# Kernel tuning notes

Measured on AMD Instinct MI355X. Metric: run time of the kernel, lower is better.

## Reference

```python
import jax, jax.numpy as jnp
import numpy as np

RHO = 1e-8
EPS = 1e-8
THRESH = 0.9
MARK = -2


def maxi(x):
    # keep only the max entry along last dim, zero elsewhere
    idx = jnp.argmax(x, axis=-1, keepdims=True)
    return jnp.where(jnp.arange(x.shape[-1]) == idx, x, 0.0)


def argmaxi(x, eps=EPS):
    mx = jnp.abs(maxi(x))
    factors = jnp.max(mx, axis=-1, keepdims=True) - eps
    return mx / factors


def outer_forward(mm0, xs, rho=RHO):
    # mm0: (fields, mems, dim), xs: (batch, fields, dim)
    m = mm0 - 0.5
    x = xs - 0.5
    num = jnp.einsum('fmd,bfd->bfm', m, x) * 0.5
    m_norm = jnp.sqrt(jnp.sum(m * m, axis=-1))            # (f, m)
    x_norm = jnp.sqrt(jnp.sum(x * x, axis=-1))[..., None]  # (b, f, 1)
    return num / (m_norm[None] * x_norm + rho) + 0.5


def hidden_forward(mm, child_x, rho=RHO):
    # mm: (nodes, children, h_mems, c_mems), child_x: (batch, nodes*children, c_mems)
    n, c, hm, cm = mm.shape
    b = child_x.shape[0]
    x = maxi(child_x).reshape(b, n, c, cm)
    prop = jnp.einsum('nchk,bnck->bnh', mm, x)
    x_norm = jnp.sqrt(jnp.sum(x * x, axis=(2, 3)))[..., None]  # (b, n, 1)
    return prop / (c * x_norm + rho)


def mark_reserved_indices(acts, usages, trigger, mark=MARK):
    # acts: (b, n, m); usages: (n, m); trigger: (b, n, 1)
    res = jnp.argsort(acts, axis=-1)[:, :, -1:]        # argmax index, (b, n, 1)
    res = jnp.where(trigger, -1, res)
    res = res[:, :, 0].T                               # (n, b)
    sort_indices = jnp.argsort(usages, axis=-1)        # (n, m) ascending usage
    mask = res != -1                                   # (n, b)
    matches = ((res[:, :, None] == sort_indices[:, None, :]) & mask[:, :, None]).any(axis=1)  # (n, m)
    return jnp.where(matches, mark, sort_indices), sort_indices


def move_value_to_back(x, value=MARK):
    order = jnp.argsort((x == value).astype(jnp.int32), axis=-1)  # stable sort
    return jnp.take_along_axis(x, order, axis=-1)


def expand_for_batches(x, batch_size):
    n, m = x.shape
    full = batch_size // m + 1
    tiled = jnp.broadcast_to(x[None], (full, n, m)).transpose(1, 0, 2).reshape(n, -1)
    return tiled[:, :batch_size]


def growth_argmaxi(x, counts, eps=EPS, threshold=THRESH):
    b, n, m = x.shape
    normal = argmaxi(x, eps)
    trigger = jnp.sum(x > threshold, axis=-1, keepdims=True) <= 0  # (b, n, 1)
    avail, allidx = mark_reserved_indices(normal, counts, trigger, MARK)
    avail = move_value_to_back(avail, MARK)
    avail = expand_for_batches(avail, b)
    allidx = expand_for_batches(allidx, b)
    final = jnp.where(avail == MARK, allidx, avail)  # (n, b)
    idx = final.T.reshape(b, n, 1)
    vals = jnp.take_along_axis(x, idx, axis=-1)
    vals = jnp.where(vals == 0, 1.0, vals)
    gp = jnp.where(jnp.arange(m) == idx, vals, 0.0)  # scatter into zeros
    gp = argmaxi(jnp.abs(gp), eps)
    grown = jnp.where(trigger, gp, normal)
    uc = jnp.sum(grown, axis=0)
    uc = jnp.where(uc <= 0, counts, uc)
    return grown, uc


def setup_inputs() -> dict:
    key = jax.random.key(0)
    k1, k2, k3, k4 = jax.random.split(key, 4)
    xs = jax.random.uniform(k1, (32, 4096, 64), dtype=jnp.float32)
    mm0 = jax.random.uniform(k2, (4096, 64, 64), dtype=jnp.float32)
    mm1 = jax.random.normal(k3, (512, 8, 64, 64), dtype=jnp.float32) * 0.1
    mm2 = jax.random.normal(k4, (64, 8, 64, 64), dtype=jnp.float32) * 0.1
    counts = jnp.ones((64, 64), dtype=jnp.float32)
    return {'xs': xs, 'mm0': mm0, 'mm1': mm1, 'mm2': mm2, 'counts': counts}


def reference(xs, mm0, mm1, mm2, counts):
    h0 = outer_forward(mm0, xs)      # (b, 4096, 64)
    h1 = hidden_forward(mm1, h0)     # (b, 512, 64)
    h2 = hidden_forward(mm2, h1)     # (b, 64, 64)
    grown, _ = growth_argmaxi(h2, counts)
    return grown
```

## Files before the change

### kernel.cpp

```cpp
#include <hip/hip_runtime.h>
#include <cstdint>
#include <cstddef>

#define RHO 1e-8f
#define EPSV 1e-8f
#define THRESH 0.9f

typedef float v2f __attribute__((ext_vector_type(2)));

__device__ __forceinline__ float wave_max(float v) {
#pragma unroll
  for (int off = 1; off < 64; off <<= 1) v = fmaxf(v, __shfl_xor(v, off, 64));
  return v;
}

__global__ __launch_bounds__(128) void stage1_kernel(
    const float* __restrict__ xs, const float* __restrict__ mm0,
    float* __restrict__ maxv1, int* __restrict__ idx1) {
  const int lane = threadIdx.x & 63;
  const int wave = threadIdx.x >> 6;
  const int f = __builtin_amdgcn_readfirstlane(blockIdx.x * 2 + wave);

  __shared__ float vbuf[2][32 * 65];
  float* vb = vbuf[wave];

  const float4* mrow =
      reinterpret_cast<const float4*>(mm0 + ((size_t)f * 64 + lane) * 64);
  v2f m2[32];
#pragma unroll
  for (int j = 0; j < 16; ++j) {
    float4 v = mrow[j];
    m2[2 * j] = (v2f){v.x - 0.5f, v.y - 0.5f};
    m2[2 * j + 1] = (v2f){v.z - 0.5f, v.w - 0.5f};
  }
  v2f mn2 = {0.f, 0.f}, sm2 = {0.f, 0.f};
#pragma unroll
  for (int j = 0; j < 32; ++j) {
    mn2 = m2[j] * m2[j] + mn2;
    sm2 = sm2 + m2[j];
  }
  const float mn = sqrtf(mn2.x + mn2.y);
  const float sm = sm2.x + sm2.y;

  float xnv;
  {
    const int b = lane & 31;
    const float4* xr =
        reinterpret_cast<const float4*>(xs + ((size_t)b * 4096 + f) * 64);
    v2f s2 = {0.f, 0.f}, s1 = {0.f, 0.f};
#pragma unroll
    for (int j = 0; j < 16; ++j) {
      float4 v = xr[j];
      v2f p0 = {v.x, v.y}, p1 = {v.z, v.w};
      s2 = p0 * p0 + s2;
      s2 = p1 * p1 + s2;
      s1 = s1 + p0 + p1;
    }
    xnv = sqrtf(s2.x + s2.y - (s1.x + s1.y) + 16.f);
  }

  const float* xf = xs + (size_t)f * 64;
#pragma clang loop unroll_count(1)
  for (int b = 0; b < 32; ++b) {
    const float4* xq = reinterpret_cast<const float4*>(xf + (size_t)b * (4096 * 64));
    const float xnb =
        __int_as_float(__builtin_amdgcn_readlane(__float_as_int(xnv), b));
    v2f a0 = {0.f, 0.f}, a1 = {0.f, 0.f}, a2 = {0.f, 0.f}, a3 = {0.f, 0.f};
#pragma unroll
    for (int j = 0; j < 16; j += 4) {
      float4 q0 = xq[j], q1 = xq[j + 1], q2 = xq[j + 2], q3 = xq[j + 3];
      a0 = m2[2 * j + 0] * (v2f){q0.x, q0.y} + a0;
      a0 = m2[2 * j + 1] * (v2f){q0.z, q0.w} + a0;
      a1 = m2[2 * j + 2] * (v2f){q1.x, q1.y} + a1;
      a1 = m2[2 * j + 3] * (v2f){q1.z, q1.w} + a1;
      a2 = m2[2 * j + 4] * (v2f){q2.x, q2.y} + a2;
      a2 = m2[2 * j + 5] * (v2f){q2.z, q2.w} + a2;
      a3 = m2[2 * j + 6] * (v2f){q3.x, q3.y} + a3;
      a3 = m2[2 * j + 7] * (v2f){q3.z, q3.w} + a3;
    }
    v2f as = (a0 + a1) + (a2 + a3);
    const float acc = as.x + as.y - 0.5f * sm;
    const float val = (acc * 0.5f) / (mn * xnb + RHO) + 0.5f;
    vb[b * 65 + lane] = val;
  }

  const int bb = lane & 31, half = lane >> 5;
  float best = -__builtin_inff();
  int bi = 0;
#pragma unroll
  for (int j = 0; j < 32; ++j) {
    float v = vb[bb * 65 + half * 32 + j];
    if (v > best) { best = v; bi = half * 32 + j; }
  }
  const float ov = __shfl_xor(best, 32, 64);
  const int oi = __shfl_xor(bi, 32, 64);
  const bool lo = (half == 0);
  const float bl = lo ? best : ov;
  const int il = lo ? bi : oi;
  const float bh = lo ? ov : best;
  const int ih = lo ? oi : bi;
  const float fb = (bl >= bh) ? bl : bh;
  const int fi = (bl >= bh) ? il : ih;
  if (lane < 32) {
    maxv1[f * 32 + lane] = fb;
    idx1[f * 32 + lane] = fi;
  }
}

__global__ __launch_bounds__(256) void stage2_kernel(
    const float* __restrict__ maxv_in, const int* __restrict__ idx_in,
    const float* __restrict__ mm,
    float* __restrict__ maxv_out, int* __restrict__ idx_out) {
  const int node = blockIdx.x;
  const int lane = threadIdx.x & 63;
  const int wave = threadIdx.x >> 6;
  const int tid = threadIdx.x;

  __shared__ float tile[4 * 4096];

  const float4* src = reinterpret_cast<const float4*>(mm + (size_t)node * (8 * 4096));

  float acc[8], s2[8];
#pragma unroll
  for (int i = 0; i < 8; ++i) { acc[i] = 0.f; s2[i] = 0.f; }

#pragma clang loop unroll_count(1)
  for (int phase = 0; phase < 2; ++phase) {
    if (phase) __syncthreads();
#pragma unroll
    for (int i = 0; i < 16; ++i) {
      int g = tid + 256 * i;
      float4 v = src[phase * 4096 + g];
      int cl = g >> 10, rem = g & 1023;
      int h = rem >> 4, k0 = (rem & 15) * 4;
      float* base = &tile[cl * 4096];
      base[(k0 + 0) * 64 + (h ^ (k0 + 0))] = v.x;
      base[(k0 + 1) * 64 + (h ^ (k0 + 1))] = v.y;
      base[(k0 + 2) * 64 + (h ^ (k0 + 2))] = v.z;
      base[(k0 + 3) * 64 + (h ^ (k0 + 3))] = v.w;
    }
    __syncthreads();
#pragma unroll
    for (int i = 0; i < 8; ++i) {
      const int b = wave * 8 + i;
#pragma unroll
      for (int cl = 0; cl < 4; ++cl) {
        const int c = phase * 4 + cl;
        const int off = __builtin_amdgcn_readfirstlane((node * 8 + c) * 32 + b);
        const int k = idx_in[off];
        const float v = maxv_in[off];
        const float w = tile[cl * 4096 + k * 64 + (lane ^ k)];
        acc[i] = fmaf(w, v, acc[i]);
        s2[i] = fmaf(v, v, s2[i]);
      }
    }
  }

#pragma unroll
  for (int i = 0; i < 8; ++i) {
    const int b = wave * 8 + i;
    const float val = acc[i] / (8.f * sqrtf(s2[i]) + RHO);
    const float mx = wave_max(val);
    unsigned long long t = __ballot(val == mx);
    int j0 = __ffsll((long long)t) - 1;
    if (lane == 0) {
      maxv_out[node * 32 + b] = mx;
      idx_out[node * 32 + b] = j0;
    }
  }
}

__global__ __launch_bounds__(256) void grow_kernel(
    const float* __restrict__ maxv_in, const int* __restrict__ idx_in,
    const float* __restrict__ mm,
    const float* __restrict__ counts, float* __restrict__ out) {
  const int node = blockIdx.x;
  const int lane = threadIdx.x & 63;
  const int wave = threadIdx.x >> 6;
  const int tid = threadIdx.x;

  __shared__ float tile[2 * 4096];
  __shared__ float hbuf[32 * 64];
  __shared__ float mxvS[32];
  __shared__ int idxS[32];
  __shared__ int trgS[32];
  __shared__ float cntS[64];
  __shared__ int sidxS[64];
  __shared__ int flagS[64];
  __shared__ int compS[64];
  __shared__ int selS[32];
  __shared__ float valS[32];
  __shared__ int keptS[1];

  const float4* src = reinterpret_cast<const float4*>(mm + (size_t)node * (8 * 4096));

  float acc[8], s2[8];
#pragma unroll
  for (int i = 0; i < 8; ++i) { acc[i] = 0.f; s2[i] = 0.f; }

#pragma clang loop unroll_count(1)
  for (int phase = 0; phase < 4; ++phase) {
    if (phase) __syncthreads();
#pragma unroll
    for (int i = 0; i < 8; ++i) {
      int g = tid + 256 * i;
      float4 v = src[phase * 2048 + g];
      int cl = g >> 10, rem = g & 1023;
      int h = rem >> 4, k0 = (rem & 15) * 4;
      float* base = &tile[cl * 4096];
      base[(k0 + 0) * 64 + (h ^ (k0 + 0))] = v.x;
      base[(k0 + 1) * 64 + (h ^ (k0 + 1))] = v.y;
      base[(k0 + 2) * 64 + (h ^ (k0 + 2))] = v.z;
      base[(k0 + 3) * 64 + (h ^ (k0 + 3))] = v.w;
    }
    __syncthreads();
#pragma unroll
    for (int i = 0; i < 8; ++i) {
      const int b = wave * 8 + i;
#pragma unroll
      for (int cl = 0; cl < 2; ++cl) {
        const int c = phase * 2 + cl;
        const int off = __builtin_amdgcn_readfirstlane((node * 8 + c) * 32 + b);
        const int k = idx_in[off];
        const float v = maxv_in[off];
        const float w = tile[cl * 4096 + k * 64 + (lane ^ k)];
        acc[i] = fmaf(w, v, acc[i]);
        s2[i] = fmaf(v, v, s2[i]);
      }
    }
  }

#pragma unroll
  for (int i = 0; i < 8; ++i) {
    const int b = wave * 8 + i;
    const float val = acc[i] / (8.f * sqrtf(s2[i]) + RHO);
    const float mx = wave_max(val);
    unsigned long long t = __ballot(val == mx);
    int j0 = __ffsll((long long)t) - 1;
    hbuf[b * 64 + lane] = val;
    unsigned long long big = __ballot(val > THRESH);
    if (lane == 0) {
      mxvS[b] = mx; idxS[b] = j0; trgS[b] = (big == 0ULL) ? 1 : 0;
    }
  }

  if (tid < 64) { cntS[tid] = counts[node * 64 + tid]; flagS[tid] = 0; }
  __syncthreads();
  if (tid < 64) {
    float cl = cntS[tid];
    int rank = 0;
    for (int j = 0; j < 64; ++j) {
      float cj = cntS[j];
      rank += (cj < cl || (cj == cl && j < tid)) ? 1 : 0;
    }
    sidxS[rank] = tid;
  }
  __syncthreads();
  if (tid < 32) {
    const int b = tid;
    if (!trgS[b]) {
      int j = idxS[b];
      float a = fabsf(mxvS[b]);
      int res;
      if (a > EPSV) res = j;
      else if (a == 0.f) res = 63;
      else if (a == EPSV) res = j;
      else res = (j == 63) ? 62 : 63;
      flagS[res] = 1;
    }
  }
  __syncthreads();
  if (wave == 0) {
    int s = sidxS[lane];
    int keep = flagS[s] ? 0 : 1;
    unsigned long long kb = __ballot(keep);
    int pos = __popcll(kb & ((1ULL << lane) - 1ULL));
    if (keep) compS[pos] = s;
    if (lane == 0) keptS[0] = __popcll(kb);
  }
  __syncthreads();
  if (tid < 32) {
    const int b = tid;
    int fin = (b < keptS[0]) ? compS[b] : sidxS[b];
    int idxb; float a;
    if (trgS[b]) {
      idxb = fin;
      float v = hbuf[b * 64 + idxb];
      if (v == 0.f) v = 1.f;
      a = fabsf(v);
    } else {
      idxb = idxS[b];
      a = fabsf(mxvS[b]);
    }
    selS[b] = idxb;
    valS[b] = a / (a - EPSV);
  }
  __syncthreads();
#pragma unroll
  for (int r = 0; r < 8; ++r) {
    int i = tid + 256 * r;
    int b = i >> 6, h = i & 63;
    out[((size_t)b * 64 + node) * 64 + h] = (h == selS[b]) ? valS[b] : 0.f;
  }
}

extern "C" void kernel_launch(void* const* d_in, const int* in_sizes, int n_in,
                              void* d_out, int out_size, void* d_ws, size_t ws_size,
                              hipStream_t stream) {
  const float* xs = (const float*)d_in[0];
  const float* mm0 = (const float*)d_in[1];
  const float* mm1 = (const float*)d_in[2];
  const float* mm2 = (const float*)d_in[3];
  const float* counts = (const float*)d_in[4];
  float* out = (float*)d_out;
  char* ws = (char*)d_ws;

  float* maxv1 = (float*)(ws + 0);
  int* idx1 = (int*)(ws + 524288);
  float* maxv2 = (float*)(ws + 1048576);
  int* idx2 = (int*)(ws + 1114112);

  stage1_kernel<<<dim3(2048), dim3(128), 0, stream>>>(xs, mm0, maxv1, idx1);
  stage2_kernel<<<dim3(512), dim3(256), 0, stream>>>(maxv1, idx1, mm1, maxv2, idx2);
  grow_kernel<<<dim3(64), dim3(256), 0, stream>>>(maxv2, idx2, mm2, counts, out);
}
```

Measured before the change: 225.2 us.

## Stage stage1 operands in LDS with register-tiled outer product; double-buffer child tiles

Stage1 now loads each field's centered memory matrix and batch vectors into padded shared memory and computes the 64x32 dot products as an 8x4 register-tiled outer product per lane, followed by a shuffle-based argmax reduction. Before, each lane held one memory row in registers and streamed every batch row from global memory. In stage2 and grow, the per-node weight staging is reworked into a register-prefetched ping-pong between two LDS tiles, one child at a time, so global loads overlap compute. The costs are higher register pressure from the 64-accumulator tile, extra LDS traffic, and a changed tie-break and precision path, since inputs are now centered before the norm is computed.

```diff
diff --git a/kernel.cpp b/kernel.cpp
--- a/kernel.cpp
+++ b/kernel.cpp
@@ -21,91 +21,153 @@
   const int wave = threadIdx.x >> 6;
   const int f = __builtin_amdgcn_readfirstlane(blockIdx.x * 2 + wave);
 
-  __shared__ float vbuf[2][32 * 65];
-  float* vb = vbuf[wave];
-
-  const float4* mrow =
-      reinterpret_cast<const float4*>(mm0 + ((size_t)f * 64 + lane) * 64);
-  v2f m2[32];
-#pragma unroll
-  for (int j = 0; j < 16; ++j) {
-    float4 v = mrow[j];
-    m2[2 * j] = (v2f){v.x - 0.5f, v.y - 0.5f};
-    m2[2 * j + 1] = (v2f){v.z - 0.5f, v.w - 0.5f};
-  }
-  v2f mn2 = {0.f, 0.f}, sm2 = {0.f, 0.f};
-#pragma unroll
-  for (int j = 0; j < 32; ++j) {
-    mn2 = m2[j] * m2[j] + mn2;
-    sm2 = sm2 + m2[j];
-  }
-  const float mn = sqrtf(mn2.x + mn2.y);
-  const float sm = sm2.x + sm2.y;
-
-  float xnv;
+  __shared__ float mbuf[2][64 * 68];
+  __shared__ float xbuf[2][32 * 68];
+  float* mb = mbuf[wave];
+  float* xb = xbuf[wave];
+
+  const float* mf = mm0 + (size_t)f * 4096;
+#pragma unroll
+  for (int i = 0; i < 16; ++i) {
+    const int g = i * 64 + lane;
+    const int r = g >> 4, dq = g & 15;
+    float4 v = *reinterpret_cast<const float4*>(mf + r * 64 + dq * 4);
+    float4 w = {v.x - 0.5f, v.y - 0.5f, v.z - 0.5f, v.w - 0.5f};
+    *reinterpret_cast<float4*>(&mb[r * 68 + dq * 4]) = w;
+  }
+  const float* xf = xs + (size_t)f * 64;
+#pragma unroll
+  for (int i = 0; i < 8; ++i) {
+    const int g = i * 64 + lane;
+    const int b = g >> 4, dq = g & 15;
+    float4 v = *reinterpret_cast<const float4*>(xf + (size_t)b * (4096 * 64) + dq * 4);
+    float4 w = {v.x - 0.5f, v.y - 0.5f, v.z - 0.5f, v.w - 0.5f};
+    *reinterpret_cast<float4*>(&xb[b * 68 + dq * 4]) = w;
+  }
+
+  float mnv, xnv;
   {
-    const int b = lane & 31;
-    const float4* xr =
-        reinterpret_cast<const float4*>(xs + ((size_t)b * 4096 + f) * 64);
-    v2f s2 = {0.f, 0.f}, s1 = {0.f, 0.f};
+    v2f s = {0.f, 0.f};
+    const float* mr = &mb[lane * 68];
 #pragma unroll
     for (int j = 0; j < 16; ++j) {
-      float4 v = xr[j];
-      v2f p0 = {v.x, v.y}, p1 = {v.z, v.w};
-      s2 = p0 * p0 + s2;
-      s2 = p1 * p1 + s2;
-      s1 = s1 + p0 + p1;
-    }
-    xnv = sqrtf(s2.x + s2.y - (s1.x + s1.y) + 16.f);
-  }
-
-  const float* xf = xs + (size_t)f * 64;
-#pragma clang loop unroll_count(1)
-  for (int b = 0; b < 32; ++b) {
-    const float4* xq = reinterpret_cast<const float4*>(xf + (size_t)b * (4096 * 64));
-    const float xnb =
-        __int_as_float(__builtin_amdgcn_readlane(__float_as_int(xnv), b));
-    v2f a0 = {0.f, 0.f}, a1 = {0.f, 0.f}, a2 = {0.f, 0.f}, a3 = {0.f, 0.f};
-#pragma unroll
-    for (int j = 0; j < 16; j += 4) {
-      float4 q0 = xq[j], q1 = xq[j + 1], q2 = xq[j + 2], q3 = xq[j + 3];
-      a0 = m2[2 * j + 0] * (v2f){q0.x, q0.y} + a0;
-      a0 = m2[2 * j + 1] * (v2f){q0.z, q0.w} + a0;
-      a1 = m2[2 * j + 2] * (v2f){q1.x, q1.y} + a1;
-      a1 = m2[2 * j + 3] * (v2f){q1.z, q1.w} + a1;
-      a2 = m2[2 * j + 4] * (v2f){q2.x, q2.y} + a2;
-      a2 = m2[2 * j + 5] * (v2f){q2.z, q2.w} + a2;
-      a3 = m2[2 * j + 6] * (v2f){q3.x, q3.y} + a3;
-      a3 = m2[2 * j + 7] * (v2f){q3.z, q3.w} + a3;
-    }
-    v2f as = (a0 + a1) + (a2 + a3);
-    const float acc = as.x + as.y - 0.5f * sm;
-    const float val = (acc * 0.5f) / (mn * xnb + RHO) + 0.5f;
-    vb[b * 65 + lane] = val;
-  }
-
-  const int bb = lane & 31, half = lane >> 5;
-  float best = -__builtin_inff();
-  int bi = 0;
-#pragma unroll
-  for (int j = 0; j < 32; ++j) {
-    float v = vb[bb * 65 + half * 32 + j];
-    if (v > best) { best = v; bi = half * 32 + j; }
-  }
-  const float ov = __shfl_xor(best, 32, 64);
-  const int oi = __shfl_xor(bi, 32, 64);
-  const bool lo = (half == 0);
-  const float bl = lo ? best : ov;
-  const int il = lo ? bi : oi;
-  const float bh = lo ? ov : best;
-  const int ih = lo ? oi : bi;
-  const float fb = (bl >= bh) ? bl : bh;
-  const int fi = (bl >= bh) ? il : ih;
-  if (lane < 32) {
-    maxv1[f * 32 + lane] = fb;
-    idx1[f * 32 + lane] = fi;
-  }
-}
+      float4 v = *reinterpret_cast<const float4*>(mr + 4 * j);
+      s = (v2f){v.x, v.y} * (v2f){v.x, v.y} + s;
+      s = (v2f){v.z, v.w} * (v2f){v.z, v.w} + s;
+    }
+    mnv = sqrtf(s.x + s.y);
+  }
+  {
+    v2f s = {0.f, 0.f};
+    const float* xr = &xb[(lane & 31) * 68];
+#pragma unroll
+    for (int j = 0; j < 16; ++j) {
+      float4 v = *reinterpret_cast<const float4*>(xr + 4 * j);
+      s = (v2f){v.x, v.y} * (v2f){v.x, v.y} + s;
+      s = (v2f){v.z, v.w} * (v2f){v.z, v.w} + s;
+    }
+    xnv = sqrtf(s.x + s.y);
+  }
+
+  const int mg = lane >> 3, bg = lane & 7;
+  v2f acc[8][4][2];
+#pragma unroll
+  for (int i = 0; i < 8; ++i)
+#pragma unroll
+    for (int j = 0; j < 4; ++j) {
+      acc[i][j][0] = (v2f){0.f, 0.f};
+      acc[i][j][1] = (v2f){0.f, 0.f};
+    }
+
+#pragma unroll
+  for (int d0 = 0; d0 < 64; d0 += 4) {
+    float4 a[8], bx[4];
+#pragma unroll
+    for (int i = 0; i < 8; ++i)
+      a[i] = *reinterpret_cast<const float4*>(&mb[(mg + 8 * i) * 68 + d0]);
+#pragma unroll
+    for (int j = 0; j < 4; ++j)
+      bx[j] = *reinterpret_cast<const float4*>(&xb[(bg + 8 * j) * 68 + d0]);
+#pragma unroll
+    for (int i = 0; i < 8; ++i)
+#pragma unroll
+      for (int j = 0; j < 4; ++j) {
+        acc[i][j][0] = (v2f){a[i].x, a[i].y} * (v2f){bx[j].x, bx[j].y} + acc[i][j][0];
+        acc[i][j][1] = (v2f){a[i].z, a[i].w} * (v2f){bx[j].z, bx[j].w} + acc[i][j][1];
+      }
+  }
+
+  float mn_i[8], xn_j[4];
+#pragma unroll
+  for (int i = 0; i < 8; ++i) mn_i[i] = __shfl(mnv, mg + 8 * i, 64);
+#pragma unroll
+  for (int j = 0; j < 4; ++j) xn_j[j] = __shfl(xnv, bg + 8 * j, 64);
+
+  float best[4];
+  int bidx[4];
+#pragma unroll
+  for (int j = 0; j < 4; ++j) { best[j] = -__builtin_inff(); bidx[j] = 0; }
+#pragma unroll
+  for (int i = 0; i < 8; ++i)
+#pragma unroll
+    for (int j = 0; j < 4; ++j) {
+      const float dot =
+          acc[i][j][0].x + acc[i][j][0].y + acc[i][j][1].x + acc[i][j][1].y;
+      const float val = (dot * 0.5f) / (mn_i[i] * xn_j[j] + RHO) + 0.5f;
+      if (val > best[j]) { best[j] = val; bidx[j] = mg + 8 * i; }
+    }
+#pragma unroll
+  for (int off = 8; off < 64; off <<= 1) {
+#pragma unroll
+    for (int j = 0; j < 4; ++j) {
+      const float pv = __shfl_xor(best[j], off, 64);
+      const int pm = __shfl_xor(bidx[j], off, 64);
+      if (pv > best[j] || (pv == best[j] && pm < bidx[j])) {
+        best[j] = pv; bidx[j] = pm;
+      }
+    }
+  }
+  if (mg == 0) {
+#pragma unroll
+    for (int j = 0; j < 4; ++j) {
+      const int b = bg + 8 * j;
+      maxv1[f * 32 + b] = best[j];
+      idx1[f * 32 + b] = bidx[j];
+    }
+  }
+}
+
+#define STAGE_WRITE(T, R)                                    \
+  do {                                                       \
+    _Pragma("unroll") for (int i_ = 0; i_ < 4; ++i_) {       \
+      const int g_ = tid + 256 * i_;                         \
+      const int h_ = g_ >> 4, k0_ = (g_ & 15) * 4;           \
+      (T)[(k0_ + 0) * 64 + (h_ ^ (k0_ + 0))] = (R)[i_].x;    \
+      (T)[(k0_ + 1) * 64 + (h_ ^ (k0_ + 1))] = (R)[i_].y;    \
+      (T)[(k0_ + 2) * 64 + (h_ ^ (k0_ + 2))] = (R)[i_].z;    \
+      (T)[(k0_ + 3) * 64 + (h_ ^ (k0_ + 3))] = (R)[i_].w;    \
+    }                                                        \
+  } while (0)
+
+#define LOAD_CHILD(R, C)                                     \
+  do {                                                       \
+    _Pragma("unroll") for (int i_ = 0; i_ < 4; ++i_)         \
+        (R)[i_] = src[(C) * 1024 + tid + 256 * i_];          \
+  } while (0)
+
+#define COMPUTE_CHILD(C, T)                                              \
+  do {                                                                   \
+    _Pragma("unroll") for (int i_ = 0; i_ < 8; ++i_) {                   \
+      const int b_ = wave * 8 + i_;                                      \
+      const int off_ =                                                   \
+          __builtin_amdgcn_readfirstlane((node * 8 + (C)) * 32 + b_);    \
+      const int k_ = idx_in[off_];                                       \
+      const float v_ = maxv_in[off_];                                    \
+      const float w_ = (T)[k_ * 64 + (lane ^ k_)];                       \
+      acc[i_] = fmaf(w_, v_, acc[i_]);                                   \
+      s2[i_] = fmaf(v_, v_, s2[i_]);                                     \
+    }                                                                    \
+  } while (0)
 
 __global__ __launch_bounds__(256) void stage2_kernel(
     const float* __restrict__ maxv_in, const int* __restrict__ idx_in,
@@ -116,7 +178,7 @@
   const int wave = threadIdx.x >> 6;
   const int tid = threadIdx.x;
 
-  __shared__ float tile[4 * 4096];
+  __shared__ float tA[4096], tB[4096];
 
   const float4* src = reinterpret_cast<const float4*>(mm + (size_t)node * (8 * 4096));
 
@@ -124,36 +186,24 @@
 #pragma unroll
   for (int i = 0; i < 8; ++i) { acc[i] = 0.f; s2[i] = 0.f; }
 
-#pragma clang loop unroll_count(1)
-  for (int phase = 0; phase < 2; ++phase) {
-    if (phase) __syncthreads();
-#pragma unroll
-    for (int i = 0; i < 16; ++i) {
-      int g = tid + 256 * i;
-      float4 v = src[phase * 4096 + g];
-      int cl = g >> 10, rem = g & 1023;
-      int h = rem >> 4, k0 = (rem & 15) * 4;
-      float* base = &tile[cl * 4096];
-      base[(k0 + 0) * 64 + (h ^ (k0 + 0))] = v.x;
-      base[(k0 + 1) * 64 + (h ^ (k0 + 1))] = v.y;
-      base[(k0 + 2) * 64 + (h ^ (k0 + 2))] = v.z;
-      base[(k0 + 3) * 64 + (h ^ (k0 + 3))] = v.w;
-    }
+  float4 rE[4], rO[4];
+  LOAD_CHILD(rE, 0);
+  LOAD_CHILD(rO, 1);
+  STAGE_WRITE(tA, rE);
+  __syncthreads();
+
+#pragma unroll
+  for (int cc = 0; cc < 8; cc += 2) {
+    if (cc + 2 < 8) LOAD_CHILD(rE, cc + 2);
+    COMPUTE_CHILD(cc, tA);
+    STAGE_WRITE(tB, rO);
     __syncthreads();
-#pragma unroll
-    for (int i = 0; i < 8; ++i) {
-      const int b = wave * 8 + i;
-#pragma unroll
-      for (int cl = 0; cl < 4; ++cl) {
-        const int c = phase * 4 + cl;
-        const int off = __builtin_amdgcn_readfirstlane((node * 8 + c) * 32 + b);
-        const int k = idx_in[off];
-        const float v = maxv_in[off];
-        const float w = tile[cl * 4096 + k * 64 + (lane ^ k)];
-        acc[i] = fmaf(w, v, acc[i]);
-        s2[i] = fmaf(v, v, s2[i]);
-      }
-    }
+    if (cc + 3 < 8) LOAD_CHILD(rO, cc + 3);
+    COMPUTE_CHILD(cc + 1, tB);
+    if (cc + 2 < 8) {
+      STAGE_WRITE(tA, rE);
+    }
+    __syncthreads();
   }
 
 #pragma unroll
@@ -179,7 +229,7 @@
   const int wave = threadIdx.x >> 6;
   const int tid = threadIdx.x;
 
-  __shared__ float tile[2 * 4096];
+  __shared__ float tA[4096], tB[4096];
   __shared__ float hbuf[32 * 64];
   __shared__ float mxvS[32];
   __shared__ int idxS[32];
@@ -198,36 +248,24 @@
 #pragma unroll
   for (int i = 0; i < 8; ++i) { acc[i] = 0.f; s2[i] = 0.f; }
 
-#pragma clang loop unroll_count(1)
-  for (int phase = 0; phase < 4; ++phase) {
-    if (phase) __syncthreads();
-#pragma unroll
-    for (int i = 0; i < 8; ++i) {
-      int g = tid + 256 * i;
-      float4 v = src[phase * 2048 + g];
-      int cl = g >> 10, rem = g & 1023;
-      int h = rem >> 4, k0 = (rem & 15) * 4;
-      float* base = &tile[cl * 4096];
-      base[(k0 + 0) * 64 + (h ^ (k0 + 0))] = v.x;
-      base[(k0 + 1) * 64 + (h ^ (k0 + 1))] = v.y;
-      base[(k0 + 2) * 64 + (h ^ (k0 + 2))] = v.z;
-      base[(k0 + 3) * 64 + (h ^ (k0 + 3))] = v.w;
-    }
+  float4 rE[4], rO[4];
+  LOAD_CHILD(rE, 0);
+  LOAD_CHILD(rO, 1);
+  STAGE_WRITE(tA, rE);
+  __syncthreads();
+
+#pragma unroll
+  for (int cc = 0; cc < 8; cc += 2) {
+    if (cc + 2 < 8) LOAD_CHILD(rE, cc + 2);
+    COMPUTE_CHILD(cc, tA);
+    STAGE_WRITE(tB, rO);
     __syncthreads();
-#pragma unroll
-    for (int i = 0; i < 8; ++i) {
-      const int b = wave * 8 + i;
-#pragma unroll
-      for (int cl = 0; cl < 2; ++cl) {
-        const int c = phase * 2 + cl;
-        const int off = __builtin_amdgcn_readfirstlane((node * 8 + c) * 32 + b);
-        const int k = idx_in[off];
-        const float v = maxv_in[off];
-        const float w = tile[cl * 4096 + k * 64 + (lane ^ k)];
-        acc[i] = fmaf(w, v, acc[i]);
-        s2[i] = fmaf(v, v, s2[i]);
-      }
-    }
+    if (cc + 3 < 8) LOAD_CHILD(rO, cc + 3);
+    COMPUTE_CHILD(cc + 1, tB);
+    if (cc + 2 < 8) {
+      STAGE_WRITE(tA, rE);
+    }
+    __syncthreads();
   }
 
 #pragma unroll
```

New measurement: 215.0 us. 1.05x faster.
